# Optimization experiments

Measured on AMD Instinct MI355X. Metric: run time of the kernel, lower is better.

Reference implementation:

```python
import jax, jax.numpy as jnp
import numpy as np

N, E, D, K, H = 100000, 1600000, 32, 3, 1


def setup_inputs() -> dict:
    key = jax.random.key(0)
    ks = jax.random.split(key, 7)
    return {
        "src": jax.random.randint(ks[0], (E,), 0, N),
        "dst": jax.random.randint(ks[1], (E,), 0, N),
        "embedding": jax.random.normal(ks[2], (N, D), jnp.float32),
        "lambda_max": jnp.full((1,), 2.0, jnp.float32),
        # ChebConv: single Linear(k*d -> d) over concatenated Chebyshev terms (shared by both calls)
        "cheb_W": jax.random.normal(ks[3], (K * D, D), jnp.float32) / np.sqrt(K * D),
        "cheb_b": jnp.zeros((D,), jnp.float32),
        # GATv2: fc_src / fc_dst Linear(d -> H*d) + attention vector (H, d)
        "gat_W_src": jax.random.normal(ks[4], (D, H * D), jnp.float32) / np.sqrt(D),
        "gat_b_src": jnp.zeros((H * D,), jnp.float32),
        "gat_W_dst": jax.random.normal(ks[5], (D, H * D), jnp.float32) / np.sqrt(D),
        "gat_b_dst": jnp.zeros((H * D,), jnp.float32),
        "gat_attn": jax.random.normal(ks[6], (H, D), jnp.float32) / np.sqrt(D),
    }


def _cheb(src, dst, feat, lam, W, b, n):
    # DGL ChebConv with lambda_max given; activation = leaky_relu (slope 0.01)
    deg = jnp.clip(jax.ops.segment_sum(jnp.ones(src.shape[0], feat.dtype), dst, num_segments=n), 1.0)
    dinv = deg[:, None] ** -0.5  # D^{-1/2}, (N,1)
    re_norm = 2.0 / lam[0]

    def unnL(f):  # D^{-1/2} A D^{-1/2} f
        return jax.ops.segment_sum((f * dinv)[src], dst, num_segments=n) * dinv

    X0 = feat
    X1 = -re_norm * unnL(X0) + X0 * (re_norm - 1.0)
    Xs = [X0, X1]
    for _ in range(2, K):
        Xi = -2.0 * re_norm * unnL(X1) + X1 * (2.0 * (re_norm - 1.0)) - X0
        Xs.append(Xi)
        X0, X1 = X1, Xi
    return jax.nn.leaky_relu(jnp.concatenate(Xs, axis=1) @ W + b, 0.01)


def _gatv2(src, dst, h, Ws, bs, Wd, bd, attn, n):
    Hh, Dd = attn.shape
    fs = (h @ Ws + bs).reshape(n, Hh, Dd)  # feat_src 'el'
    fd = (h @ Wd + bd).reshape(n, Hh, Dd)  # feat_dst 'er'
    e = jax.nn.leaky_relu(fs[src] + fd[dst], 0.2)        # (E,H,D), GATv2 negative_slope=0.2
    logits = jnp.einsum('ehd,hd->eh', e, attn)           # (E,H)
    m = jax.ops.segment_max(logits, dst, num_segments=n)  # per-dst softmax (edge_softmax)
    ex = jnp.exp(logits - m[dst])
    a = ex / jax.ops.segment_sum(ex, dst, num_segments=n)[dst]
    ft = jax.ops.segment_sum(fs[src] * a[..., None], dst, num_segments=n)  # (N,H,D)
    return jax.nn.leaky_relu(ft, 0.01)  # activation=F.leaky_relu


def reference(src, dst, embedding, lambda_max, cheb_W, cheb_b,
              gat_W_src, gat_b_src, gat_W_dst, gat_b_dst, gat_attn):
    n, d = embedding.shape
    h = _cheb(src, dst, embedding, lambda_max, cheb_W, cheb_b, n)
    h = _cheb(src, dst, h, lambda_max, cheb_W, cheb_b, n)
    out = _gatv2(src, dst, h, gat_W_src, gat_b_src, gat_W_dst, gat_b_dst, gat_attn, n)
    return out.reshape(-1, d)
```

## Files before the change

kernel.cpp:

```cpp
#include <hip/hip_runtime.h>

#define TPB 256
#define NB 512
#define CAPB 4096
#define CHUNK 4096

__global__ void k_zero_u(unsigned int* p, int n){
  int i = blockIdx.x*TPB + threadIdx.x;
  if(i < n) p[i] = 0u;
}

__global__ __launch_bounds__(TPB) void k_bin1(const int* __restrict__ src,
    const int* __restrict__ dst,
    unsigned int* __restrict__ btail, unsigned int* __restrict__ binned,
    int E, int npb){
  __shared__ unsigned int hist[NB];
  __shared__ unsigned int lofs[NB];
  __shared__ unsigned int base[NB];
  __shared__ unsigned int s[TPB];
  __shared__ int2 stage[CHUNK];
  int t = threadIdx.x;
  for(int i = t; i < NB; i += TPB) hist[i] = 0u;
  __syncthreads();
  int e0 = blockIdx.x*CHUNK;
  int e1 = e0 + CHUNK; if(e1 > E) e1 = E;
  for(int e = e0 + t; e < e1; e += TPB)
    atomicAdd(&hist[dst[e]/npb], 1u);
  __syncthreads();
  unsigned int a0 = hist[2*t], a1 = hist[2*t+1];
  unsigned int tsum = a0 + a1;
  s[t] = tsum; __syncthreads();
  for(int off = 1; off < TPB; off <<= 1){
    unsigned int x = (t >= off) ? s[t - off] : 0u;
    __syncthreads();
    s[t] += x;
    __syncthreads();
  }
  unsigned int excl = s[t] - tsum;
  lofs[2*t]   = excl;
  lofs[2*t+1] = excl + a0;
  base[2*t]   = a0 ? atomicAdd(btail + 2*t,   a0) : 0u;
  base[2*t+1] = a1 ? atomicAdd(btail + 2*t+1, a1) : 0u;
  __syncthreads();
  hist[2*t]   = lofs[2*t];
  hist[2*t+1] = lofs[2*t+1];
  __syncthreads();
  for(int e = e0 + t; e < e1; e += TPB){
    int d = dst[e];
    int b = d / npb;
    unsigned int p = atomicAdd(&hist[b], 1u);
    stage[p] = make_int2(src[e], d);
  }
  __syncthreads();
  int tot = e1 - e0;
  for(int i = t; i < tot; i += TPB){
    int2 sd = stage[i];
    int b = sd.y / npb;
    unsigned int go = base[b] + ((unsigned)i - lofs[b]);
    if(go < (unsigned)CAPB)
      binned[(size_t)b*CAPB + go] = ((unsigned)sd.x << 8) | (unsigned)(sd.y - b*npb);
  }
}

__global__ __launch_bounds__(TPB) void k_scanb(const unsigned int* __restrict__ btail,
    unsigned int* __restrict__ bbase, unsigned int* __restrict__ ptr, int N, int E){
  __shared__ unsigned int s[TPB];
  __shared__ unsigned int carry;
  int t = threadIdx.x;
  if(t == 0) carry = 0u;
  __syncthreads();
  for(int base = 0; base < NB; base += TPB){
    unsigned int v = btail[base + t];
    s[t] = v; __syncthreads();
    for(int off = 1; off < TPB; off <<= 1){
      unsigned int x = (t >= off) ? s[t - off] : 0u;
      __syncthreads();
      s[t] += x;
      __syncthreads();
    }
    bbase[base + t] = s[t] - v + carry;
    __syncthreads();
    if(t == 0) carry += s[TPB-1];
    __syncthreads();
  }
  if(t == 0) ptr[N] = (unsigned int)E;
}

__global__ __launch_bounds__(TPB) void k_bin2x(const unsigned int* __restrict__ binned,
    const unsigned int* __restrict__ btail, const unsigned int* __restrict__ bbase,
    unsigned int* __restrict__ ptr, float* __restrict__ dinv,
    int* __restrict__ csr, int npb, int N){
  __shared__ unsigned int ebuf[CAPB];
  __shared__ int obuf[CAPB];
  __shared__ unsigned int cnt_s[256];
  __shared__ unsigned int s[TPB];
  __shared__ unsigned int curs[256];
  int b = blockIdx.x;
  int n0 = b*npb; if(n0 >= N) return;
  int t = threadIdx.x;
  unsigned int cnt = btail[b]; if(cnt > (unsigned)CAPB) cnt = CAPB;
  unsigned int segbase = bbase[b];
  cnt_s[t] = 0u;
  __syncthreads();
  for(unsigned int i = t; i < cnt; i += TPB){
    unsigned int e = binned[(size_t)b*CAPB + i];
    ebuf[i] = e;
    atomicAdd(&cnt_s[e & 255u], 1u);
  }
  __syncthreads();
  unsigned int v = cnt_s[t];
  s[t] = v; __syncthreads();
  for(int off = 1; off < TPB; off <<= 1){
    unsigned int x = (t >= off) ? s[t - off] : 0u;
    __syncthreads();
    s[t] += x;
    __syncthreads();
  }
  unsigned int lo = s[t] - v;
  int n = n0 + t;
  if(t < npb && n < N){
    ptr[n]  = segbase + lo;
    dinv[n] = 1.0f / sqrtf(fmaxf((float)v, 1.0f));
  }
  curs[t] = lo;
  __syncthreads();
  for(unsigned int i = t; i < cnt; i += TPB){
    unsigned int e = ebuf[i];
    unsigned int p = atomicAdd(&curs[e & 255u], 1u);
    obuf[p] = (int)(e >> 8);
  }
  __syncthreads();
  for(unsigned int i = t; i < cnt; i += TPB)
    csr[segbase + i] = obuf[i];
}

__device__ __forceinline__ float4 agg_gather4(const unsigned int* __restrict__ ptr,
    const int* __restrict__ csr,
    const float* __restrict__ X, const float* __restrict__ dinv, int t, int lane){
  int g  = lane >> 3;
  int f4 = (lane & 7) << 2;
  unsigned int p0 = ptr[t], p1 = ptr[t+1];
  float4 S0 = make_float4(0.f,0.f,0.f,0.f);
  float4 S1 = make_float4(0.f,0.f,0.f,0.f);
  for(unsigned int base = p0; base < p1; base += 32){
    int idx = 0; float dva = 0.f;
    unsigned int pos = base + (unsigned)lane;
    if(pos < p1){ idx = csr[pos]; dva = dinv[idx]; }
    unsigned int cnt = p1 - base; if(cnt > 32u) cnt = 32u;
    unsigned int rounds = (cnt + 3u) >> 2;
    for(unsigned int r = 0; r < rounds; r += 2){
      int el0 = (int)(r << 2) + g;
      int s0  = __shfl(idx, el0, 32);
      float d0 = __shfl(dva, el0, 32);
      const float4 x0 = *(const float4*)(X + (size_t)s0*32 + f4);
      if(r + 1 < rounds){
        int el1 = el0 + 4;
        int s1  = __shfl(idx, el1, 32);
        float d1 = __shfl(dva, el1, 32);
        const float4 x1 = *(const float4*)(X + (size_t)s1*32 + f4);
        S1.x += x1.x*d1; S1.y += x1.y*d1; S1.z += x1.z*d1; S1.w += x1.w*d1;
      }
      S0.x += x0.x*d0; S0.y += x0.y*d0; S0.z += x0.z*d0; S0.w += x0.w*d0;
    }
  }
  float4 S;
  S.x = S0.x + S1.x; S.y = S0.y + S1.y; S.z = S0.z + S1.z; S.w = S0.w + S1.w;
  S.x += __shfl_xor(S.x, 8, 32);  S.y += __shfl_xor(S.y, 8, 32);
  S.z += __shfl_xor(S.z, 8, 32);  S.w += __shfl_xor(S.w, 8, 32);
  S.x += __shfl_xor(S.x, 16, 32); S.y += __shfl_xor(S.y, 16, 32);
  S.z += __shfl_xor(S.z, 16, 32); S.w += __shfl_xor(S.w, 16, 32);
  return S;
}

__global__ __launch_bounds__(TPB) void k_cheb1(const unsigned int* __restrict__ ptr,
    const int* __restrict__ csr,
    const float* __restrict__ X0, const float* __restrict__ dinv,
    const float* __restrict__ lam, float* __restrict__ X1, int N){
  int t = blockIdx.x*8 + (threadIdx.x >> 5);
  if(t >= N) return;
  int lane = threadIdx.x & 31;
  float4 S = agg_gather4(ptr, csr, X0, dinv, t, lane);
  if((lane >> 3) != 0) return;
  int f4 = (lane & 7) << 2;
  float re = 2.0f / lam[0];
  float dt = dinv[t];
  size_t o = (size_t)t*32 + f4;
  const float4 x0 = *(const float4*)(X0 + o);
  float4 r;
  r.x = -re*(S.x*dt) + (re-1.0f)*x0.x;
  r.y = -re*(S.y*dt) + (re-1.0f)*x0.y;
  r.z = -re*(S.z*dt) + (re-1.0f)*x0.z;
  r.w = -re*(S.w*dt) + (re-1.0f)*x0.w;
  *(float4*)(X1 + o) = r;
}

__global__ __launch_bounds__(TPB) void k_cheb2(const unsigned int* __restrict__ ptr,
    const int* __restrict__ csr,
    const float* __restrict__ X0, const float* __restrict__ X1,
    const float* __restrict__ dinv, const float* __restrict__ lam,
    float* __restrict__ X2, int N){
  int t = blockIdx.x*8 + (threadIdx.x >> 5);
  if(t >= N) return;
  int lane = threadIdx.x & 31;
  float4 S = agg_gather4(ptr, csr, X1, dinv, t, lane);
  if((lane >> 3) != 0) return;
  int f4 = (lane & 7) << 2;
  float re = 2.0f / lam[0];
  float dt = dinv[t];
  size_t o = (size_t)t*32 + f4;
  const float4 x0 = *(const float4*)(X0 + o);
  const float4 x1 = *(const float4*)(X1 + o);
  float c1 = -2.0f*re, c2 = 2.0f*(re-1.0f);
  float4 r;
  r.x = c1*(S.x*dt) + c2*x1.x - x0.x;
  r.y = c1*(S.y*dt) + c2*x1.y - x0.y;
  r.z = c1*(S.z*dt) + c2*x1.z - x0.z;
  r.w = c1*(S.w*dt) + c2*x1.w - x0.w;
  *(float4*)(X2 + o) = r;
}

__global__ __launch_bounds__(TPB) void k_lin(const float* __restrict__ X0,
    const float* __restrict__ X1,
    const float* __restrict__ X2, const float* __restrict__ W,
    const float* __restrict__ b, float* __restrict__ out, int N){
  int n = blockIdx.x*TPB + threadIdx.x;
  if(n >= N) return;
  float acc[32];
  #pragma unroll
  for(int c = 0; c < 32; c++) acc[c] = b[c];
  const float* xs0 = X0 + (size_t)n*32;
  const float* xs1 = X1 + (size_t)n*32;
  const float* xs2 = X2 + (size_t)n*32;
  #pragma unroll
  for(int s3 = 0; s3 < 3; s3++){
    const float4* xp = (const float4*)(s3 == 0 ? xs0 : (s3 == 1 ? xs1 : xs2));
    #pragma unroll
    for(int q = 0; q < 8; q++){
      float4 xv = xp[q];
      const float* Wr = W + (size_t)(s3*32 + q*4)*32;
      #pragma unroll
      for(int c = 0; c < 32; c++)
        acc[c] += xv.x*Wr[c] + xv.y*Wr[32+c] + xv.z*Wr[64+c] + xv.w*Wr[96+c];
    }
  }
  float4* op = (float4*)(out + (size_t)n*32);
  #pragma unroll
  for(int q = 0; q < 8; q++){
    float4 v;
    float a;
    a = acc[4*q+0]; v.x = a > 0.f ? a : 0.01f*a;
    a = acc[4*q+1]; v.y = a > 0.f ? a : 0.01f*a;
    a = acc[4*q+2]; v.z = a > 0.f ? a : 0.01f*a;
    a = acc[4*q+3]; v.w = a > 0.f ? a : 0.01f*a;
    op[q] = v;
  }
}

__global__ __launch_bounds__(TPB) void k_fc(const float* __restrict__ h,
    const float* __restrict__ Wsr, const float* __restrict__ bsr,
    const float* __restrict__ Wds, const float* __restrict__ bds,
    float* __restrict__ fs, float* __restrict__ fd, int N){
  int n = blockIdx.x*TPB + threadIdx.x;
  if(n >= N) return;
  float as[32], ad[32];
  #pragma unroll
  for(int c = 0; c < 32; c++){ as[c] = bsr[c]; ad[c] = bds[c]; }
  const float4* xp = (const float4*)(h + (size_t)n*32);
  #pragma unroll
  for(int q = 0; q < 8; q++){
    float4 xv = xp[q];
    const float* Wr = Wsr + (size_t)(q*4)*32;
    const float* Vr = Wds + (size_t)(q*4)*32;
    #pragma unroll
    for(int c = 0; c < 32; c++){
      as[c] += xv.x*Wr[c] + xv.y*Wr[32+c] + xv.z*Wr[64+c] + xv.w*Wr[96+c];
      ad[c] += xv.x*Vr[c] + xv.y*Vr[32+c] + xv.z*Vr[64+c] + xv.w*Vr[96+c];
    }
  }
  float4* sp = (float4*)(fs + (size_t)n*32);
  float4* dp = (float4*)(fd + (size_t)n*32);
  #pragma unroll
  for(int q = 0; q < 8; q++){
    float4 v1, v2;
    v1.x = as[4*q+0]; v1.y = as[4*q+1]; v1.z = as[4*q+2]; v1.w = as[4*q+3];
    v2.x = ad[4*q+0]; v2.y = ad[4*q+1]; v2.z = ad[4*q+2]; v2.w = ad[4*q+3];
    sp[q] = v1;
    dp[q] = v2;
  }
}

__global__ __launch_bounds__(TPB) void k_gat(const unsigned int* __restrict__ ptr,
    const int* __restrict__ csr,
    const float* __restrict__ fs, const float* __restrict__ fd,
    const float* __restrict__ attn, float* __restrict__ out, int N){
  int t = blockIdx.x*8 + (threadIdx.x >> 5);
  if(t >= N) return;
  int lane = threadIdx.x & 31;
  int g  = lane >> 3;
  int f4 = (lane & 7) << 2;
  unsigned int p0 = ptr[t], p1 = ptr[t+1];
  const float4 fd4 = *(const float4*)(fd + (size_t)t*32 + f4);
  const float4 at4 = *(const float4*)(attn + f4);
  float m = -3.402823466e38f, den = 0.f;
  float4 acc = make_float4(0.f,0.f,0.f,0.f);
  for(unsigned int base = p0; base < p1; base += 32){
    int idx = 0;
    unsigned int pos = base + (unsigned)lane;
    if(pos < p1) idx = csr[pos];
    unsigned int cnt = p1 - base; if(cnt > 32u) cnt = 32u;
    unsigned int rounds = (cnt + 3u) >> 2;
    for(unsigned int r = 0; r < rounds; r++){
      int el = (int)(r << 2) + g;
      int s  = __shfl(idx, el, 32);
      const float4 f = *(const float4*)(fs + (size_t)s*32 + f4);
      float vx = f.x + fd4.x; vx = vx > 0.f ? vx : 0.2f*vx;
      float vy = f.y + fd4.y; vy = vy > 0.f ? vy : 0.2f*vy;
      float vz = f.z + fd4.z; vz = vz > 0.f ? vz : 0.2f*vz;
      float vw = f.w + fd4.w; vw = vw > 0.f ? vw : 0.2f*vw;
      float pl = vx*at4.x + vy*at4.y + vz*at4.z + vw*at4.w;
      pl += __shfl_xor(pl, 4, 32);
      pl += __shfl_xor(pl, 2, 32);
      pl += __shfl_xor(pl, 1, 32);
      if(el < (int)cnt){
        float mn = fmaxf(m, pl);
        float sc = __expf(m - mn);
        float e  = __expf(pl - mn);
        den = den*sc + e;
        acc.x = acc.x*sc + f.x*e;
        acc.y = acc.y*sc + f.y*e;
        acc.z = acc.z*sc + f.z*e;
        acc.w = acc.w*sc + f.w*e;
        m = mn;
      }
    }
  }
  #pragma unroll
  for(int off = 8; off <= 16; off <<= 1){
    float mo = __shfl_xor(m, off, 32);
    float do_ = __shfl_xor(den, off, 32);
    float ax = __shfl_xor(acc.x, off, 32);
    float ay = __shfl_xor(acc.y, off, 32);
    float az = __shfl_xor(acc.z, off, 32);
    float aw = __shfl_xor(acc.w, off, 32);
    float mn = fmaxf(m, mo);
    float a = __expf(m - mn), b = __expf(mo - mn);
    den = den*a + do_*b;
    acc.x = acc.x*a + ax*b;
    acc.y = acc.y*a + ay*b;
    acc.z = acc.z*a + az*b;
    acc.w = acc.w*a + aw*b;
    m = mn;
  }
  if(g != 0) return;
  float4 o = make_float4(0.f,0.f,0.f,0.f);
  if(den > 0.f){
    float inv = 1.0f / den;
    o.x = acc.x*inv; o.x = o.x > 0.f ? o.x : 0.01f*o.x;
    o.y = acc.y*inv; o.y = o.y > 0.f ? o.y : 0.01f*o.y;
    o.z = acc.z*inv; o.z = o.z > 0.f ? o.z : 0.01f*o.z;
    o.w = acc.w*inv; o.w = o.w > 0.f ? o.w : 0.01f*o.w;
  }
  *(float4*)(out + (size_t)t*32 + f4) = o;
}

extern "C" void kernel_launch(void* const* d_in, const int* in_sizes, int n_in,
                              void* d_out, int out_size, void* d_ws, size_t ws_size,
                              hipStream_t stream){
  const int*   src = (const int*)d_in[0];
  const int*   dst = (const int*)d_in[1];
  const float* emb = (const float*)d_in[2];
  const float* lam = (const float*)d_in[3];
  const float* cW  = (const float*)d_in[4];
  const float* cB  = (const float*)d_in[5];
  const float* gWs = (const float*)d_in[6];
  const float* gbs = (const float*)d_in[7];
  const float* gWd = (const float*)d_in[8];
  const float* gbd = (const float*)d_in[9];
  const float* gat = (const float*)d_in[10];
  const int E  = in_sizes[0];
  const int N  = in_sizes[2] / 32;
  const int NF = N * 32;
  const int npb = (N + NB - 1) / NB;

  int gN  = (N + TPB-1)/TPB;
  int gR  = (N + 7)/8;
  int gB1 = (E + CHUNK-1)/CHUNK;

  char* p = (char*)d_ws;
  auto alloc = [&](size_t bytes)->char*{ char* r = p; p += (bytes + 255) & ~(size_t)255; return r; };
  unsigned int* ptrA = (unsigned int*)alloc((size_t)(N+1)*4);
  unsigned int* btail= (unsigned int*)alloc((size_t)NB*4);
  unsigned int* bbase= (unsigned int*)alloc((size_t)NB*4);
  float* dinv = (float*)alloc((size_t)N*4);
  int*   csr  = (int*)alloc((size_t)E*4);
  float* X1   = (float*)alloc((size_t)NF*4);
  float* X2   = (float*)alloc((size_t)NF*4);
  float* h1   = (float*)alloc((size_t)NF*4);
  float* h2   = (float*)alloc((size_t)NF*4);
  unsigned int* binned = (unsigned int*)X1;

  k_zero_u<<<(NB+TPB-1)/TPB, TPB, 0, stream>>>(btail, NB);
  k_bin1<<<gB1, TPB, 0, stream>>>(src, dst, btail, binned, E, npb);
  k_scanb<<<1, TPB, 0, stream>>>(btail, bbase, ptrA, N, E);
  k_bin2x<<<NB, TPB, 0, stream>>>(binned, btail, bbase, ptrA, dinv, csr, npb, N);

  k_cheb1<<<gR, TPB, 0, stream>>>(ptrA, csr, emb, dinv, lam, X1, N);
  k_cheb2<<<gR, TPB, 0, stream>>>(ptrA, csr, emb, X1, dinv, lam, X2, N);
  k_lin<<<gN, TPB, 0, stream>>>(emb, X1, X2, cW, cB, h1, N);

  k_cheb1<<<gR, TPB, 0, stream>>>(ptrA, csr, h1, dinv, lam, X1, N);
  k_cheb2<<<gR, TPB, 0, stream>>>(ptrA, csr, h1, X1, dinv, lam, X2, N);
  k_lin<<<gN, TPB, 0, stream>>>(h1, X1, X2, cW, cB, h2, N);

  k_fc<<<gN, TPB, 0, stream>>>(h2, gWs, gbs, gWd, gbd, X1 , X2 , N);
  k_gat<<<gR, TPB, 0, stream>>>(ptrA, csr, X1, X2, gat, (float*)d_out, N);
}
```

Measured before the change: 376.4 us.

## Prescale features by dinv and split Chebyshev gathers into feature chunks

Producer kernels (bin2x, cheb1, lin) now also write copies of their outputs pre-multiplied by D^{-1/2}. The aggregation therefore no longer loads dinv per neighbor or multiplies by it. The gather is also restructured: each of four blocks per node group handles an 8-float column chunk, with 16 edges in flight per warp, so each pass touches a smaller slice of the feature table, which may fit the cache better. In exchange there are extra full-size buffers to write, and the CSR index list and edge pointers are read four times.

```diff
diff --git a/kernel.cpp b/kernel.cpp
--- a/kernel.cpp
+++ b/kernel.cpp
@@ -89,7 +89,8 @@
 __global__ __launch_bounds__(TPB) void k_bin2x(const unsigned int* __restrict__ binned,
     const unsigned int* __restrict__ btail, const unsigned int* __restrict__ bbase,
     unsigned int* __restrict__ ptr, float* __restrict__ dinv,
-    int* __restrict__ csr, int npb, int N){
+    int* __restrict__ csr, const float* __restrict__ emb,
+    float* __restrict__ emb_s, int npb, int N){
   __shared__ unsigned int ebuf[CAPB];
   __shared__ int obuf[CAPB];
   __shared__ unsigned int cnt_s[256];
@@ -132,59 +133,69 @@
   __syncthreads();
   for(unsigned int i = t; i < cnt; i += TPB)
     csr[segbase + i] = obuf[i];
-}
-
-__device__ __forceinline__ float4 agg_gather4(const unsigned int* __restrict__ ptr,
-    const int* __restrict__ csr,
-    const float* __restrict__ X, const float* __restrict__ dinv, int t, int lane){
-  int g  = lane >> 3;
-  int f4 = (lane & 7) << 2;
+  int nn = npb; if(n0 + nn > N) nn = N - n0;
+  for(int i = t; i < nn*8; i += TPB){
+    int node = i >> 3;
+    float dv = 1.0f / sqrtf(fmaxf((float)cnt_s[node], 1.0f));
+    size_t o = (size_t)(n0 + node)*32 + ((i & 7) << 2);
+    const float4 e4 = *(const float4*)(emb + o);
+    float4 r; r.x = e4.x*dv; r.y = e4.y*dv; r.z = e4.z*dv; r.w = e4.w*dv;
+    *(float4*)(emb_s + o) = r;
+  }
+}
+
+__device__ __forceinline__ float4 agg_chunk(const unsigned int* __restrict__ ptr,
+    const int* __restrict__ csr, const float* __restrict__ Xs,
+    int t, int lane, int off){
+  int sub = lane >> 1;
   unsigned int p0 = ptr[t], p1 = ptr[t+1];
   float4 S0 = make_float4(0.f,0.f,0.f,0.f);
   float4 S1 = make_float4(0.f,0.f,0.f,0.f);
   for(unsigned int base = p0; base < p1; base += 32){
-    int idx = 0; float dva = 0.f;
+    int idx = 0;
     unsigned int pos = base + (unsigned)lane;
-    if(pos < p1){ idx = csr[pos]; dva = dinv[idx]; }
+    if(pos < p1) idx = csr[pos];
     unsigned int cnt = p1 - base; if(cnt > 32u) cnt = 32u;
-    unsigned int rounds = (cnt + 3u) >> 2;
-    for(unsigned int r = 0; r < rounds; r += 2){
-      int el0 = (int)(r << 2) + g;
-      int s0  = __shfl(idx, el0, 32);
-      float d0 = __shfl(dva, el0, 32);
-      const float4 x0 = *(const float4*)(X + (size_t)s0*32 + f4);
-      if(r + 1 < rounds){
-        int el1 = el0 + 4;
-        int s1  = __shfl(idx, el1, 32);
-        float d1 = __shfl(dva, el1, 32);
-        const float4 x1 = *(const float4*)(X + (size_t)s1*32 + f4);
-        S1.x += x1.x*d1; S1.y += x1.y*d1; S1.z += x1.z*d1; S1.w += x1.w*d1;
-      }
-      S0.x += x0.x*d0; S0.y += x0.y*d0; S0.z += x0.z*d0; S0.w += x0.w*d0;
-    }
+    int s0 = __shfl(idx, sub, 32);
+    float w0 = (sub < (int)cnt) ? 1.f : 0.f;
+    const float4 x0 = *(const float4*)(Xs + (size_t)s0*32 + off);
+    if(cnt > 16u){
+      int s1 = __shfl(idx, 16 + sub, 32);
+      float w1 = (16 + sub < (int)cnt) ? 1.f : 0.f;
+      const float4 x1 = *(const float4*)(Xs + (size_t)s1*32 + off);
+      S1.x += x1.x*w1; S1.y += x1.y*w1; S1.z += x1.z*w1; S1.w += x1.w*w1;
+    }
+    S0.x += x0.x*w0; S0.y += x0.y*w0; S0.z += x0.z*w0; S0.w += x0.w*w0;
   }
   float4 S;
   S.x = S0.x + S1.x; S.y = S0.y + S1.y; S.z = S0.z + S1.z; S.w = S0.w + S1.w;
-  S.x += __shfl_xor(S.x, 8, 32);  S.y += __shfl_xor(S.y, 8, 32);
-  S.z += __shfl_xor(S.z, 8, 32);  S.w += __shfl_xor(S.w, 8, 32);
-  S.x += __shfl_xor(S.x, 16, 32); S.y += __shfl_xor(S.y, 16, 32);
-  S.z += __shfl_xor(S.z, 16, 32); S.w += __shfl_xor(S.w, 16, 32);
+  #pragma unroll
+  for(int d = 2; d <= 16; d <<= 1){
+    S.x += __shfl_xor(S.x, d, 32);
+    S.y += __shfl_xor(S.y, d, 32);
+    S.z += __shfl_xor(S.z, d, 32);
+    S.w += __shfl_xor(S.w, d, 32);
+  }
   return S;
 }
 
-__global__ __launch_bounds__(TPB) void k_cheb1(const unsigned int* __restrict__ ptr,
-    const int* __restrict__ csr,
+__global__ __launch_bounds__(TPB) void k_cheb1c(const unsigned int* __restrict__ ptr,
+    const int* __restrict__ csr, const float* __restrict__ Xs,
     const float* __restrict__ X0, const float* __restrict__ dinv,
-    const float* __restrict__ lam, float* __restrict__ X1, int N){
-  int t = blockIdx.x*8 + (threadIdx.x >> 5);
+    const float* __restrict__ lam, float* __restrict__ X1,
+    float* __restrict__ X1s, int N, int nbR){
+  int bid = blockIdx.x;
+  int c   = bid / nbR;
+  int rb  = bid - c*nbR;
+  int t = rb*8 + (threadIdx.x >> 5);
   if(t >= N) return;
   int lane = threadIdx.x & 31;
-  float4 S = agg_gather4(ptr, csr, X0, dinv, t, lane);
-  if((lane >> 3) != 0) return;
-  int f4 = (lane & 7) << 2;
+  int off = (c << 3) + ((lane & 1) << 2);
+  float4 S = agg_chunk(ptr, csr, Xs, t, lane, off);
+  if((lane >> 1) != 0) return;
   float re = 2.0f / lam[0];
   float dt = dinv[t];
-  size_t o = (size_t)t*32 + f4;
+  size_t o = (size_t)t*32 + off;
   const float4 x0 = *(const float4*)(X0 + o);
   float4 r;
   r.x = -re*(S.x*dt) + (re-1.0f)*x0.x;
@@ -192,22 +203,27 @@
   r.z = -re*(S.z*dt) + (re-1.0f)*x0.z;
   r.w = -re*(S.w*dt) + (re-1.0f)*x0.w;
   *(float4*)(X1 + o) = r;
-}
-
-__global__ __launch_bounds__(TPB) void k_cheb2(const unsigned int* __restrict__ ptr,
-    const int* __restrict__ csr,
+  float4 rs; rs.x = r.x*dt; rs.y = r.y*dt; rs.z = r.z*dt; rs.w = r.w*dt;
+  *(float4*)(X1s + o) = rs;
+}
+
+__global__ __launch_bounds__(TPB) void k_cheb2c(const unsigned int* __restrict__ ptr,
+    const int* __restrict__ csr, const float* __restrict__ Xs,
     const float* __restrict__ X0, const float* __restrict__ X1,
     const float* __restrict__ dinv, const float* __restrict__ lam,
-    float* __restrict__ X2, int N){
-  int t = blockIdx.x*8 + (threadIdx.x >> 5);
+    float* __restrict__ X2, int N, int nbR){
+  int bid = blockIdx.x;
+  int c   = bid / nbR;
+  int rb  = bid - c*nbR;
+  int t = rb*8 + (threadIdx.x >> 5);
   if(t >= N) return;
   int lane = threadIdx.x & 31;
-  float4 S = agg_gather4(ptr, csr, X1, dinv, t, lane);
-  if((lane >> 3) != 0) return;
-  int f4 = (lane & 7) << 2;
+  int off = (c << 3) + ((lane & 1) << 2);
+  float4 S = agg_chunk(ptr, csr, Xs, t, lane, off);
+  if((lane >> 1) != 0) return;
   float re = 2.0f / lam[0];
   float dt = dinv[t];
-  size_t o = (size_t)t*32 + f4;
+  size_t o = (size_t)t*32 + off;
   const float4 x0 = *(const float4*)(X0 + o);
   const float4 x1 = *(const float4*)(X1 + o);
   float c1 = -2.0f*re, c2 = 2.0f*(re-1.0f);
@@ -222,7 +238,8 @@
 __global__ __launch_bounds__(TPB) void k_lin(const float* __restrict__ X0,
     const float* __restrict__ X1,
     const float* __restrict__ X2, const float* __restrict__ W,
-    const float* __restrict__ b, float* __restrict__ out, int N){
+    const float* __restrict__ b, const float* __restrict__ dinv,
+    float* __restrict__ out, float* __restrict__ outs, int N){
   int n = blockIdx.x*TPB + threadIdx.x;
   if(n >= N) return;
   float acc[32];
@@ -243,7 +260,9 @@
         acc[c] += xv.x*Wr[c] + xv.y*Wr[32+c] + xv.z*Wr[64+c] + xv.w*Wr[96+c];
     }
   }
+  float dv = dinv[n];
   float4* op = (float4*)(out + (size_t)n*32);
+  float4* osp = (float4*)(outs ? outs + (size_t)n*32 : nullptr);
   #pragma unroll
   for(int q = 0; q < 8; q++){
     float4 v;
@@ -253,6 +272,10 @@
     a = acc[4*q+2]; v.z = a > 0.f ? a : 0.01f*a;
     a = acc[4*q+3]; v.w = a > 0.f ? a : 0.01f*a;
     op[q] = v;
+    if(outs){
+      float4 vs; vs.x = v.x*dv; vs.y = v.y*dv; vs.z = v.z*dv; vs.w = v.w*dv;
+      osp[q] = vs;
+    }
   }
 }
 
@@ -383,7 +406,9 @@
   const int npb = (N + NB - 1) / NB;
 
   int gN  = (N + TPB-1)/TPB;
-  int gR  = (N + 7)/8;
+  int nbR = (N + 7)/8;
+  int gC  = 4*nbR;
+  int gR  = nbR;
   int gB1 = (E + CHUNK-1)/CHUNK;
 
   char* p = (char*)d_ws;
@@ -397,20 +422,23 @@
   float* X2   = (float*)alloc((size_t)NF*4);
   float* h1   = (float*)alloc((size_t)NF*4);
   float* h2   = (float*)alloc((size_t)NF*4);
+  float* embs = (float*)alloc((size_t)NF*4);
+  float* X1s  = (float*)alloc((size_t)NF*4);
+  float* h1s  = (float*)alloc((size_t)NF*4);
   unsigned int* binned = (unsigned int*)X1;
 
   k_zero_u<<<(NB+TPB-1)/TPB, TPB, 0, stream>>>(btail, NB);
   k_bin1<<<gB1, TPB, 0, stream>>>(src, dst, btail, binned, E, npb);
   k_scanb<<<1, TPB, 0, stream>>>(btail, bbase, ptrA, N, E);
-  k_bin2x<<<NB, TPB, 0, stream>>>(binned, btail, bbase, ptrA, dinv, csr, npb, N);
-
-  k_cheb1<<<gR, TPB, 0, stream>>>(ptrA, csr, emb, dinv, lam, X1, N);
-  k_cheb2<<<gR, TPB, 0, stream>>>(ptrA, csr, emb, X1, dinv, lam, X2, N);
-  k_lin<<<gN, TPB, 0, stream>>>(emb, X1, X2, cW, cB, h1, N);
-
-  k_cheb1<<<gR, TPB, 0, stream>>>(ptrA, csr, h1, dinv, lam, X1, N);
-  k_cheb2<<<gR, TPB, 0, stream>>>(ptrA, csr, h1, X1, dinv, lam, X2, N);
-  k_lin<<<gN, TPB, 0, stream>>>(h1, X1, X2, cW, cB, h2, N);
+  k_bin2x<<<NB, TPB, 0, stream>>>(binned, btail, bbase, ptrA, dinv, csr, emb, embs, npb, N);
+
+  k_cheb1c<<<gC, TPB, 0, stream>>>(ptrA, csr, embs, emb, dinv, lam, X1, X1s, N, nbR);
+  k_cheb2c<<<gC, TPB, 0, stream>>>(ptrA, csr, X1s, emb, X1, dinv, lam, X2, N, nbR);
+  k_lin<<<gN, TPB, 0, stream>>>(emb, X1, X2, cW, cB, dinv, h1, h1s, N);
+
+  k_cheb1c<<<gC, TPB, 0, stream>>>(ptrA, csr, h1s, h1, dinv, lam, X1, X1s, N, nbR);
+  k_cheb2c<<<gC, TPB, 0, stream>>>(ptrA, csr, X1s, h1, X1, dinv, lam, X2, N, nbR);
+  k_lin<<<gN, TPB, 0, stream>>>(h1, X1, X2, cW, cB, dinv, h2, nullptr, N);
 
   k_fc<<<gN, TPB, 0, stream>>>(h2, gWs, gbs, gWd, gbd, X1 , X2 , N);
   k_gat<<<gR, TPB, 0, stream>>>(ptrA, csr, X1, X2, gat, (float*)d_out, N);
```

New measurement: 887.0 us. +135.6%, slower.

## Pre-scale features by D^-1/2 to drop per-edge dinv gathers in aggregation

Applied to the files above, without the earlier changes.

Source features are now multiplied by dinv once per node and stored in separate buffers. The scaling is fused into k_bin2x for the embedding and into k_cheb1 for X1, and a new k_scale kernel handles h1. The gather loop then reads only csr indices and the pre-scaled rows, which removes the dependent per-edge random load of dinv[idx] and its shuffle. In exchange it writes and reads extra N×32 float buffers, adds one kernel launch, and makes the embedding-scaling path in k_bin2x depend on cnt_s holding per-node counts.

```diff
diff --git a/kernel.cpp b/kernel.cpp
--- a/kernel.cpp
+++ b/kernel.cpp
@@ -89,7 +89,8 @@
 __global__ __launch_bounds__(TPB) void k_bin2x(const unsigned int* __restrict__ binned,
     const unsigned int* __restrict__ btail, const unsigned int* __restrict__ bbase,
     unsigned int* __restrict__ ptr, float* __restrict__ dinv,
-    int* __restrict__ csr, int npb, int N){
+    int* __restrict__ csr, const float* __restrict__ emb,
+    float* __restrict__ emb_s, int npb, int N){
   __shared__ unsigned int ebuf[CAPB];
   __shared__ int obuf[CAPB];
   __shared__ unsigned int cnt_s[256];
@@ -132,35 +133,53 @@
   __syncthreads();
   for(unsigned int i = t; i < cnt; i += TPB)
     csr[segbase + i] = obuf[i];
-}
-
-__device__ __forceinline__ float4 agg_gather4(const unsigned int* __restrict__ ptr,
-    const int* __restrict__ csr,
-    const float* __restrict__ X, const float* __restrict__ dinv, int t, int lane){
+  int nn = npb; if(n0 + nn > N) nn = N - n0;
+  for(int i = t; i < nn*8; i += TPB){
+    int node = i >> 3;
+    float dv = 1.0f / sqrtf(fmaxf((float)cnt_s[node], 1.0f));
+    size_t o = (size_t)(n0 + node)*32 + ((i & 7) << 2);
+    const float4 e4 = *(const float4*)(emb + o);
+    float4 r; r.x = e4.x*dv; r.y = e4.y*dv; r.z = e4.z*dv; r.w = e4.w*dv;
+    *(float4*)(emb_s + o) = r;
+  }
+}
+
+__global__ __launch_bounds__(TPB) void k_scale(const float* __restrict__ x,
+    const float* __restrict__ dinv, float* __restrict__ xs, int N){
+  int i = blockIdx.x*TPB + threadIdx.x;
+  if(i >= N*8) return;
+  float dv = dinv[i >> 3];
+  const float4 v = ((const float4*)x)[i];
+  float4 r; r.x = v.x*dv; r.y = v.y*dv; r.z = v.z*dv; r.w = v.w*dv;
+  ((float4*)xs)[i] = r;
+}
+
+__device__ __forceinline__ float4 agg_gather4s(const unsigned int* __restrict__ ptr,
+    const int* __restrict__ csr, const float* __restrict__ Xs, int t, int lane){
   int g  = lane >> 3;
   int f4 = (lane & 7) << 2;
   unsigned int p0 = ptr[t], p1 = ptr[t+1];
   float4 S0 = make_float4(0.f,0.f,0.f,0.f);
   float4 S1 = make_float4(0.f,0.f,0.f,0.f);
   for(unsigned int base = p0; base < p1; base += 32){
-    int idx = 0; float dva = 0.f;
+    int idx = 0;
     unsigned int pos = base + (unsigned)lane;
-    if(pos < p1){ idx = csr[pos]; dva = dinv[idx]; }
+    if(pos < p1) idx = csr[pos];
     unsigned int cnt = p1 - base; if(cnt > 32u) cnt = 32u;
     unsigned int rounds = (cnt + 3u) >> 2;
     for(unsigned int r = 0; r < rounds; r += 2){
       int el0 = (int)(r << 2) + g;
       int s0  = __shfl(idx, el0, 32);
-      float d0 = __shfl(dva, el0, 32);
-      const float4 x0 = *(const float4*)(X + (size_t)s0*32 + f4);
+      float w0 = (el0 < (int)cnt) ? 1.f : 0.f;
+      const float4 x0 = *(const float4*)(Xs + (size_t)s0*32 + f4);
       if(r + 1 < rounds){
         int el1 = el0 + 4;
         int s1  = __shfl(idx, el1, 32);
-        float d1 = __shfl(dva, el1, 32);
-        const float4 x1 = *(const float4*)(X + (size_t)s1*32 + f4);
-        S1.x += x1.x*d1; S1.y += x1.y*d1; S1.z += x1.z*d1; S1.w += x1.w*d1;
+        float w1 = (el1 < (int)cnt) ? 1.f : 0.f;
+        const float4 x1 = *(const float4*)(Xs + (size_t)s1*32 + f4);
+        S1.x += x1.x*w1; S1.y += x1.y*w1; S1.z += x1.z*w1; S1.w += x1.w*w1;
       }
-      S0.x += x0.x*d0; S0.y += x0.y*d0; S0.z += x0.z*d0; S0.w += x0.w*d0;
+      S0.x += x0.x*w0; S0.y += x0.y*w0; S0.z += x0.z*w0; S0.w += x0.w*w0;
     }
   }
   float4 S;
@@ -173,13 +192,14 @@
 }
 
 __global__ __launch_bounds__(TPB) void k_cheb1(const unsigned int* __restrict__ ptr,
-    const int* __restrict__ csr,
+    const int* __restrict__ csr, const float* __restrict__ Xs,
     const float* __restrict__ X0, const float* __restrict__ dinv,
-    const float* __restrict__ lam, float* __restrict__ X1, int N){
+    const float* __restrict__ lam, float* __restrict__ X1,
+    float* __restrict__ X1s, int N){
   int t = blockIdx.x*8 + (threadIdx.x >> 5);
   if(t >= N) return;
   int lane = threadIdx.x & 31;
-  float4 S = agg_gather4(ptr, csr, X0, dinv, t, lane);
+  float4 S = agg_gather4s(ptr, csr, Xs, t, lane);
   if((lane >> 3) != 0) return;
   int f4 = (lane & 7) << 2;
   float re = 2.0f / lam[0];
@@ -192,17 +212,19 @@
   r.z = -re*(S.z*dt) + (re-1.0f)*x0.z;
   r.w = -re*(S.w*dt) + (re-1.0f)*x0.w;
   *(float4*)(X1 + o) = r;
+  float4 rs; rs.x = r.x*dt; rs.y = r.y*dt; rs.z = r.z*dt; rs.w = r.w*dt;
+  *(float4*)(X1s + o) = rs;
 }
 
 __global__ __launch_bounds__(TPB) void k_cheb2(const unsigned int* __restrict__ ptr,
-    const int* __restrict__ csr,
+    const int* __restrict__ csr, const float* __restrict__ Xs,
     const float* __restrict__ X0, const float* __restrict__ X1,
     const float* __restrict__ dinv, const float* __restrict__ lam,
     float* __restrict__ X2, int N){
   int t = blockIdx.x*8 + (threadIdx.x >> 5);
   if(t >= N) return;
   int lane = threadIdx.x & 31;
-  float4 S = agg_gather4(ptr, csr, X1, dinv, t, lane);
+  float4 S = agg_gather4s(ptr, csr, Xs, t, lane);
   if((lane >> 3) != 0) return;
   int f4 = (lane & 7) << 2;
   float re = 2.0f / lam[0];
@@ -384,6 +406,7 @@
 
   int gN  = (N + TPB-1)/TPB;
   int gR  = (N + 7)/8;
+  int gS  = (N*8 + TPB-1)/TPB;
   int gB1 = (E + CHUNK-1)/CHUNK;
 
   char* p = (char*)d_ws;
@@ -397,19 +420,23 @@
   float* X2   = (float*)alloc((size_t)NF*4);
   float* h1   = (float*)alloc((size_t)NF*4);
   float* h2   = (float*)alloc((size_t)NF*4);
+  float* embs = (float*)alloc((size_t)NF*4);
+  float* X1s  = (float*)alloc((size_t)NF*4);
+  float* h1s  = (float*)alloc((size_t)NF*4);
   unsigned int* binned = (unsigned int*)X1;
 
   k_zero_u<<<(NB+TPB-1)/TPB, TPB, 0, stream>>>(btail, NB);
   k_bin1<<<gB1, TPB, 0, stream>>>(src, dst, btail, binned, E, npb);
   k_scanb<<<1, TPB, 0, stream>>>(btail, bbase, ptrA, N, E);
-  k_bin2x<<<NB, TPB, 0, stream>>>(binned, btail, bbase, ptrA, dinv, csr, npb, N);
-
-  k_cheb1<<<gR, TPB, 0, stream>>>(ptrA, csr, emb, dinv, lam, X1, N);
-  k_cheb2<<<gR, TPB, 0, stream>>>(ptrA, csr, emb, X1, dinv, lam, X2, N);
+  k_bin2x<<<NB, TPB, 0, stream>>>(binned, btail, bbase, ptrA, dinv, csr, emb, embs, npb, N);
+
+  k_cheb1<<<gR, TPB, 0, stream>>>(ptrA, csr, embs, emb, dinv, lam, X1, X1s, N);
+  k_cheb2<<<gR, TPB, 0, stream>>>(ptrA, csr, X1s, emb, X1, dinv, lam, X2, N);
   k_lin<<<gN, TPB, 0, stream>>>(emb, X1, X2, cW, cB, h1, N);
-
-  k_cheb1<<<gR, TPB, 0, stream>>>(ptrA, csr, h1, dinv, lam, X1, N);
-  k_cheb2<<<gR, TPB, 0, stream>>>(ptrA, csr, h1, X1, dinv, lam, X2, N);
+  k_scale<<<gS, TPB, 0, stream>>>(h1, dinv, h1s, N);
+
+  k_cheb1<<<gR, TPB, 0, stream>>>(ptrA, csr, h1s, h1, dinv, lam, X1, X1s, N);
+  k_cheb2<<<gR, TPB, 0, stream>>>(ptrA, csr, X1s, h1, X1, dinv, lam, X2, N);
   k_lin<<<gN, TPB, 0, stream>>>(h1, X1, X2, cW, cB, h2, N);
 
   k_fc<<<gN, TPB, 0, stream>>>(h2, gWs, gbs, gWd, gbd, X1 , X2 , N);
```

Result: slower. 391.2 us (+3.9%).
